# Performance work log

Measured on AMD Instinct MI355X. Metric: run time of the kernel, lower is better.

The kernel has to match this reference:

```python
import jax, jax.numpy as jnp
import numpy as np

MARGIN = 1.0
ALPHA = 0.5
EPS = 1e-12  # sqrt-smoothing epsilon (keeps grads finite on the zero diagonal)


def _pairwise_d2(x):
    # x: [B, D] -> squared euclidean distance matrix [B, B]
    sq = jnp.sum(x * x, axis=-1)
    return jnp.maximum(sq[:, None] + sq[None, :] - 2.0 * (x @ x.T), 0.0)


def setup_inputs() -> dict:
    key = jax.random.key(0)
    k1, k2 = jax.random.split(key)
    N, B, D = 32, 1024, 1024
    outputs = jax.random.normal(k1, (N, B, D), dtype=jnp.float32)
    encode_sentences = jax.random.normal(k2, (B, D), dtype=jnp.float32)
    return {"outputs": outputs, "encode_sentences": encode_sentences}


def reference(outputs, encode_sentences):
    # outputs: [N, B, D] (N secrets, batch B, embed D); encode_sentences: [B, D]
    N, B, D = outputs.shape

    # --- sentence (distance-consistency) loss ---
    # original: mean_i MSE( pdist(outputs[i]), pdist(encode_sentences) )
    d_sent = jnp.sqrt(_pairwise_d2(encode_sentences) + EPS)          # [B, B]
    d_out = jnp.sqrt(jax.vmap(_pairwise_d2)(outputs) + EPS)          # [N, B, B]
    # mean over N of per-i means == global mean (all terms same size B*B)
    sentence_loss = jnp.mean((d_out - d_sent[None]) ** 2)

    # --- secret (pairwise margin) loss ---
    # original: sum_{i<j} mean_b relu(margin - ||outputs[i,b] - outputs[j,b]||)
    x = jnp.swapaxes(outputs, 0, 1)                                   # [B, N, D]
    sq = jnp.sum(x * x, axis=-1)                                      # [B, N]
    gram = jnp.einsum('bnd,bmd->bnm', x, x)                           # [B, N, N]
    d2 = jnp.maximum(sq[:, :, None] + sq[:, None, :] - 2.0 * gram, 0.0)
    d = jnp.sqrt(d2 + EPS)                                            # [B, N, N]
    hinge = jax.nn.relu(MARGIN - d)                                   # [B, N, N]
    upper = jnp.triu(jnp.ones((N, N), dtype=bool), k=1)               # i < j mask
    secret_distance = jnp.sum(jnp.where(upper[None], hinge, 0.0)) / B
    n_pairs = N * (N - 1) / 2.0
    secret_loss = secret_distance / n_pairs

    loss = ALPHA * sentence_loss + (1.0 - ALPHA) * secret_loss
    return (loss, sentence_loss, secret_loss)
```

## Files before the change

kernel.cpp:

```cpp
#include <hip/hip_runtime.h>
#include <hip/hip_bf16.h>

#define N_SEC 32
#define BDIM 1024
#define DDIM 1024

typedef __attribute__((ext_vector_type(8))) short bf16x8;
typedef __attribute__((ext_vector_type(4))) float f32x4;
typedef __attribute__((ext_vector_type(4))) int i32x4;

#define WAITVM(n) asm volatile("s_waitcnt vmcnt(" #n ")" ::: "memory")

__device__ __forceinline__ void pipe_barrier() {
    __builtin_amdgcn_s_barrier();
    asm volatile("" ::: "memory");
    __builtin_amdgcn_sched_barrier(0);
}

__device__ __forceinline__ unsigned pk2(float a, float b) {
    union { __hip_bfloat162 h; unsigned u; } cv;
    cv.h = __float22bfloat162_rn(make_float2(a, b));
    return cv.u;
}

__device__ __forceinline__ i32x4 pack8(float4 a, float4 b) {
    i32x4 r;
    r[0] = pk2(a.x, a.y); r[1] = pk2(a.z, a.w);
    r[2] = pk2(b.x, b.y); r[3] = pk2(b.z, b.w);
    return r;
}

__device__ __forceinline__ f32x4 mfma16(bf16x8 a, bf16x8 b, f32x4 c) {
    return __builtin_amdgcn_mfma_f32_16x16x32_bf16(a, b, c, 0, 0, 0);
}

__device__ __forceinline__ float wave_sum(float v) {
    #pragma unroll
    for (int off = 32; off > 0; off >>= 1) v += __shfl_down(v, off, 64);
    return v;
}

__device__ __forceinline__ void gload16(const unsigned short* g, unsigned short* l) {
    __builtin_amdgcn_global_load_lds(
        (const __attribute__((address_space(1))) unsigned int*)g,
        (__attribute__((address_space(3))) unsigned int*)l, 16, 0, 0);
}


__global__ void prep_k(const float* __restrict__ outp, const float* __restrict__ enc,
                       unsigned short* __restrict__ Xb, unsigned short* __restrict__ Eb,
                       float* __restrict__ sq_out, float* __restrict__ sq_enc) {
    int wid = threadIdx.x >> 6, l = threadIdx.x & 63;
    int r = blockIdx.x * 4 + wid;
    bool isOut = r < N_SEC * BDIM;
    const float* src = isOut ? (outp + (size_t)r * DDIM)
                             : (enc + (size_t)(r - N_SEC * BDIM) * DDIM);
    unsigned short* dst = isOut ? (Xb + (size_t)r * DDIM)
                                : (Eb + (size_t)(r - N_SEC * BDIM) * DDIM);
    const float4* s4 = (const float4*)src;
    float s = 0.f;
    #pragma unroll
    for (int h = 0; h < 2; ++h) {
        int c = l + h * 64;
        float4 v0 = s4[2 * c], v1 = s4[2 * c + 1];
        i32x4 p = pack8(v0, v1);
        *(i32x4*)&dst[c * 8] = p;
        #pragma unroll
        for (int e = 0; e < 4; ++e) {
            unsigned u = (unsigned)p[e];
            float a = __uint_as_float(u << 16);
            float b = __uint_as_float(u & 0xFFFF0000u);
            s += a * a + b * b;
        }
    }
    s = wave_sum(s);
    if (l == 0) { if (isOut) sq_out[r] = s; else sq_enc[r - N_SEC * BDIM] = s; }
}

template<int MODE>
__global__ void gram5_k(const unsigned short* __restrict__ Xb, const float* __restrict__ sqv,
                        const float* __restrict__ dsent_r, float* __restrict__ dsent_w,
                        float* __restrict__ partials) {
    int n, tile;
    if (MODE == 1) {
        int g = blockIdx.x;
        int xcd = g & 7, local = g >> 3;
        n = xcd * 4 + local / 36;
        tile = local % 36;
    } else { n = 0; tile = blockIdx.x; }
    int idx = tile, ti = 0;
    while (idx >= 8 - ti) { idx -= 8 - ti; ti++; }
    int tj = ti + idx;
    const unsigned short* Xn = Xb + (size_t)n * BDIM * DDIM;
    const float* sqn = sqv + n * BDIM;
    int i0 = ti * 128, j0 = tj * 128;
    bool diag = (ti == tj);

    __shared__ __align__(16) unsigned short Ash[3][4096];
    __shared__ __align__(16) unsigned short Bsh[3][4096];
    __shared__ float red[4];

    int t = threadIdx.x, wid = t >> 6, l = t & 63;
    int wr = wid >> 1, wc = wid & 1;
    bool dead = diag && (wr > wc);
    int cg = l >> 4, lr = l & 15;

    f32x4 acc[4][4];
    #pragma unroll
    for (int a = 0; a < 4; a++)
        #pragma unroll
        for (int c = 0; c < 4; c++) acc[a][c] = f32x4{0.f, 0.f, 0.f, 0.f};

    int eoffA[4], eoffB[4];
    #pragma unroll
    for (int f = 0; f < 4; f++) {
        int ra = wr * 64 + f * 16 + lr;
        eoffA[f] = ra * 32 + ((cg ^ ((ra >> 1) & 3)) * 8);
        int rb = wc * 64 + f * 16 + lr;
        eoffB[f] = rb * 32 + ((cg ^ ((rb >> 1) & 3)) * 8);
    }

    int rs = wid * 16 + (l >> 2);
    int cgs = (l & 3) ^ ((rs >> 1) & 3);
    const unsigned short* gA0 = Xn + (size_t)(i0 + rs) * DDIM + cgs * 8;
    const unsigned short* gA1 = gA0 + (size_t)64 * DDIM;
    const unsigned short* gB0 = Xn + (size_t)(j0 + rs) * DDIM + cgs * 8;
    const unsigned short* gB1 = gB0 + (size_t)64 * DDIM;

    auto stage = [&](int buf, int kt) {
        int ko = kt * 32;
        gload16(gA0 + ko, &Ash[buf][wid * 512]);
        gload16(gA1 + ko, &Ash[buf][2048 + wid * 512]);
        gload16(gB0 + ko, &Bsh[buf][wid * 512]);
        gload16(gB1 + ko, &Bsh[buf][2048 + wid * 512]);
    };
    auto compute = [&](int buf) {
        if (dead) return;
        bf16x8 af[4], bfr[4];
        #pragma unroll
        for (int f = 0; f < 4; f++) {
            af[f]  = *(const bf16x8*)&Ash[buf][eoffA[f]];
            bfr[f] = *(const bf16x8*)&Bsh[buf][eoffB[f]];
        }
        #pragma unroll
        for (int fi = 0; fi < 4; fi++)
            #pragma unroll
            for (int fj = 0; fj < 4; fj++) {
                if (diag && wr == wc && fj < fi) continue;
                acc[fi][fj] = mfma16(af[fi], bfr[fj], acc[fi][fj]);
            }
    };

#define GSTEP(NB, CB) do {                       \
        pipe_barrier();                          \
        int nx = c + 2; if (nx > 31) nx = 31;    \
        stage(NB, nx);                           \
        WAITVM(8);                               \
        compute(CB);                             \
        ++c; } while (0)

    stage(0, 0); stage(1, 1);
    int c = 0;
    #pragma unroll 1
    for (int it = 0; it < 10; ++it) {
        GSTEP(2, 0);
        GSTEP(0, 1);
        GSTEP(1, 2);
    }
    GSTEP(2, 0);
    GSTEP(0, 1);
#undef GSTEP
    asm volatile("s_waitcnt vmcnt(0)" ::: "memory");

    float lsum = 0.f;
    if (!dead) {
        #pragma unroll
        for (int fi = 0; fi < 4; fi++) {
            #pragma unroll
            for (int fj = 0; fj < 4; fj++) {
                if (diag && wr == wc && fj < fi) continue;
                int jg = j0 + wc * 64 + fj * 16 + lr;
                #pragma unroll
                for (int e = 0; e < 4; e++) {
                    int ig = i0 + wr * 64 + fi * 16 + cg * 4 + e;
                    float g = acc[fi][fj][e];
                    float d2 = sqn[ig] + sqn[jg] - 2.f * g;
                    float d = sqrtf(fmaxf(d2, 0.f) + 1e-12f);
                    if (MODE == 0) {
                        dsent_w[(size_t)ig * BDIM + jg] = d;
                    } else {
                        if (!diag || jg > ig) {
                            float diff = d - dsent_r[(size_t)ig * BDIM + jg];
                            lsum += diff * diff;
                        }
                    }
                }
            }
        }
    }
    if (MODE == 1) {
        lsum = wave_sum(lsum * 2.f);
        if (l == 0) red[wid] = lsum;
        __syncthreads();
        if (t == 0) partials[blockIdx.x] = red[0] + red[1] + red[2] + red[3];
    }
}

__global__ void secret4_k(const unsigned short* __restrict__ Xb,
                          const float* __restrict__ sq_out, float* __restrict__ partials) {
    __shared__ __align__(16) unsigned short S[2][32 * 4 * 128];
    __shared__ float red[4];
    int t = threadIdx.x, wid = t >> 6, l = t & 63;
    int b0 = blockIdx.x * 4;
    int cg = l >> 4, lr = l & 15;
    f32x4 a00 = {0.f,0.f,0.f,0.f}, a01 = {0.f,0.f,0.f,0.f}, a11 = {0.f,0.f,0.f,0.f};

    auto stage = [&](int buf, int kt) {
        #pragma unroll
        for (int m = 0; m < 8; ++m) {
            int n = m * 4 + wid;
            gload16(Xb + ((size_t)(n * BDIM + b0 + cg)) * DDIM + kt * 128 + ((lr ^ (n & 7)) * 8),
                    &S[buf][n * 512]);
        }
    };
    auto compute = [&](int buf) {
        #pragma unroll
        for (int k2 = 0; k2 < 4; ++k2) {
            int cs = k2 * 4 + cg;
            int cl = (cs ^ (lr & 7)) * 8;
            bf16x8 u0 = *(const bf16x8*)&S[buf][lr * 512 + wid * 128 + cl];
            bf16x8 u1 = *(const bf16x8*)&S[buf][(16 + lr) * 512 + wid * 128 + cl];
            a00 = mfma16(u0, u0, a00);
            a01 = mfma16(u0, u1, a01);
            a11 = mfma16(u1, u1, a11);
        }
    };

    stage(0, 0);
    __syncthreads();
    for (int kt = 0; kt < 6; kt += 2) {
        stage(1, kt + 1);
        compute(0);
        __syncthreads();
        stage(0, kt + 2);
        compute(1);
        __syncthreads();
    }
    stage(1, 7);
    compute(0);
    __syncthreads();
    compute(1);

    float lsum = 0.f;
    int b = b0 + wid;
    auto proc = [&](const f32x4& acc, int rb, int cb) {
        #pragma unroll
        for (int e = 0; e < 4; e++) {
            int i = rb * 16 + cg * 4 + e;
            int j = cb * 16 + lr;
            if (j > i) {
                float d2 = sq_out[(size_t)i * BDIM + b] + sq_out[(size_t)j * BDIM + b] - 2.f * acc[e];
                float d = sqrtf(fmaxf(d2, 0.f) + 1e-12f);
                lsum += fmaxf(1.f - d, 0.f);
            }
        }
    };
    proc(a00, 0, 0); proc(a01, 0, 1); proc(a11, 1, 1);
    lsum = wave_sum(lsum);
    if (l == 0) red[wid] = lsum;
    __syncthreads();
    if (t == 0) partials[blockIdx.x] = red[0] + red[1] + red[2] + red[3];
}

__global__ void fin2_k(const float* __restrict__ ps, const float* __restrict__ psec,
                       float* __restrict__ out) {
    __shared__ float red[16];
    int t = threadIdx.x;
    float s = 0.f;
    for (int i = t; i < 36 * N_SEC; i += 256) s += ps[i];
    float s2 = psec[t];
    s = wave_sum(s);
    s2 = wave_sum(s2);
    if ((t & 63) == 0) { red[t >> 6] = s; red[8 + (t >> 6)] = s2; }
    __syncthreads();
    if (t == 0) {
        float a = red[0] + red[1] + red[2] + red[3];
        float b = red[8] + red[9] + red[10] + red[11];
        float sl = a * (1.0f / 33554432.0f);
        float sec = b * (1.0f / (1024.0f * 496.0f));
        out[0] = 0.5f * sl + 0.5f * sec;
        out[1] = sl;
        out[2] = sec;
    }
}


__global__ void norms_k(const float* __restrict__ outp, const float* __restrict__ enc,
                        float* __restrict__ sq_out, float* __restrict__ sq_enc) {
    int wid = threadIdx.x >> 6, l = threadIdx.x & 63;
    int r = blockIdx.x * 4 + wid;
    const float* src = (r < N_SEC * BDIM) ? (outp + (size_t)r * DDIM)
                                          : (enc + (size_t)(r - N_SEC * BDIM) * DDIM);
    float s = 0.f;
    #pragma unroll
    for (int q = 0; q < 4; q++) {
        float4 v = reinterpret_cast<const float4*>(src)[l + q * 64];
        unsigned u0 = pk2(v.x, v.y), u1 = pk2(v.z, v.w);
        float a = __uint_as_float(u0 << 16), b = __uint_as_float(u0 & 0xFFFF0000u);
        float c = __uint_as_float(u1 << 16), d = __uint_as_float(u1 & 0xFFFF0000u);
        s += a * a + b * b + c * c + d * d;
    }
    s = wave_sum(s);
    if (l == 0) { if (r < N_SEC * BDIM) sq_out[r] = s; else sq_enc[r - N_SEC * BDIM] = s; }
}

template<int MODE>
__global__ void gram_k(const float* __restrict__ X, const float* __restrict__ sqv,
                       const float* __restrict__ dsent_r, float* __restrict__ dsent_w,
                       float* __restrict__ accum) {
    int idx = blockIdx.x, ti = 0;
    while (idx >= 8 - ti) { idx -= 8 - ti; ti++; }
    int tj = ti + idx;
    int n = (MODE == 1) ? blockIdx.y : 0;
    const float* Xn = X + (size_t)n * BDIM * DDIM;
    const float* sqn = sqv + n * BDIM;
    int i0 = ti * 128, j0 = tj * 128;
    bool diag = (ti == tj);
    __shared__ __align__(16) unsigned short Ash[128 * 32];
    __shared__ __align__(16) unsigned short Bsh[128 * 32];
    int t = threadIdx.x, wid = t >> 6, l = t & 63;
    int wr = wid >> 1, wc = wid & 1;
    bool dead = diag && (wr > wc);
    int cg = l >> 4, lr = l & 15;
    f32x4 acc[4][4];
    #pragma unroll
    for (int a = 0; a < 4; a++)
        #pragma unroll
        for (int c = 0; c < 4; c++) acc[a][c] = f32x4{0.f, 0.f, 0.f, 0.f};
    int r0 = t >> 2, c0 = t & 3;
    int swz0 = (c0 ^ (r0 & 3)) * 8;
    int off0 = r0 * 32 + swz0;
    int off1 = (r0 + 64) * 32 + swz0;
    for (int kt = 0; kt < DDIM / 32; ++kt) {
        int k0 = kt * 32;
        const float4* pa0 = (const float4*)(Xn + (size_t)(i0 + r0) * DDIM + k0 + c0 * 8);
        const float4* pa1 = (const float4*)(Xn + (size_t)(i0 + r0 + 64) * DDIM + k0 + c0 * 8);
        const float4* pb0 = (const float4*)(Xn + (size_t)(j0 + r0) * DDIM + k0 + c0 * 8);
        const float4* pb1 = (const float4*)(Xn + (size_t)(j0 + r0 + 64) * DDIM + k0 + c0 * 8);
        float4 a00 = pa0[0], a01 = pa0[1];
        float4 a10 = pa1[0], a11 = pa1[1];
        float4 b00 = pb0[0], b01 = pb0[1];
        float4 b10 = pb1[0], b11 = pb1[1];
        __syncthreads();
        *(i32x4*)&Ash[off0] = pack8(a00, a01);
        *(i32x4*)&Ash[off1] = pack8(a10, a11);
        *(i32x4*)&Bsh[off0] = pack8(b00, b01);
        *(i32x4*)&Bsh[off1] = pack8(b10, b11);
        __syncthreads();
        if (!dead) {
            bf16x8 af[4], bfr[4];
            #pragma unroll
            for (int f = 0; f < 4; f++) {
                int ra = wr * 64 + f * 16 + lr;
                af[f] = *(const bf16x8*)&Ash[ra * 32 + ((cg ^ (ra & 3)) * 8)];
                int rb = wc * 64 + f * 16 + lr;
                bfr[f] = *(const bf16x8*)&Bsh[rb * 32 + ((cg ^ (rb & 3)) * 8)];
            }
            #pragma unroll
            for (int fi = 0; fi < 4; fi++)
                #pragma unroll
                for (int fj = 0; fj < 4; fj++) {
                    if (diag && wr == wc && fj < fi) continue;
                    acc[fi][fj] = mfma16(af[fi], bfr[fj], acc[fi][fj]);
                }
        }
    }
    if (!dead) {
        float lsum = 0.f;
        #pragma unroll
        for (int fi = 0; fi < 4; fi++) {
            #pragma unroll
            for (int fj = 0; fj < 4; fj++) {
                if (diag && wr == wc && fj < fi) continue;
                int jg = j0 + wc * 64 + fj * 16 + lr;
                #pragma unroll
                for (int e = 0; e < 4; e++) {
                    int ig = i0 + wr * 64 + fi * 16 + cg * 4 + e;
                    float g = acc[fi][fj][e];
                    float d2 = sqn[ig] + sqn[jg] - 2.f * g;
                    float d = sqrtf(fmaxf(d2, 0.f) + 1e-12f);
                    if (MODE == 0) {
                        dsent_w[(size_t)ig * BDIM + jg] = d;
                    } else {
                        if (!diag || jg > ig) {
                            float diff = d - dsent_r[(size_t)ig * BDIM + jg];
                            lsum += diff * diff;
                        }
                    }
                }
            }
        }
        if (MODE == 1) {
            lsum = wave_sum(lsum * 2.f);
            if (l == 0) atomicAdd(accum, lsum);
        }
    }
}

__global__ void secret_k(const float* __restrict__ X, const float* __restrict__ sq_out,
                         float* __restrict__ accum) {
    int wid = threadIdx.x >> 6, l = threadIdx.x & 63;
    int b = blockIdx.x * 4 + wid;
    int cg = l >> 4, lr = l & 15;
    f32x4 a00 = {0.f,0.f,0.f,0.f}, a01 = {0.f,0.f,0.f,0.f}, a11 = {0.f,0.f,0.f,0.f};
    for (int kt = 0; kt < 32; ++kt) {
        int k0 = kt * 32 + cg * 8;
        const float4* p0 = (const float4*)(X + ((size_t)lr * BDIM + b) * DDIM + k0);
        const float4* p1 = (const float4*)(X + ((size_t)(16 + lr) * BDIM + b) * DDIM + k0);
        union { i32x4 i; bf16x8 s; } u0, u1;
        u0.i = pack8(p0[0], p0[1]);
        u1.i = pack8(p1[0], p1[1]);
        a00 = mfma16(u0.s, u0.s, a00);
        a01 = mfma16(u0.s, u1.s, a01);
        a11 = mfma16(u1.s, u1.s, a11);
    }
    float lsum = 0.f;
    auto proc = [&](const f32x4& acc, int rb, int cb) {
        #pragma unroll
        for (int e = 0; e < 4; e++) {
            int i = rb * 16 + cg * 4 + e;
            int j = cb * 16 + lr;
            if (j > i) {
                float d2 = sq_out[(size_t)i * BDIM + b] + sq_out[(size_t)j * BDIM + b] - 2.f * acc[e];
                float d = sqrtf(fmaxf(d2, 0.f) + 1e-12f);
                lsum += fmaxf(1.f - d, 0.f);
            }
        }
    };
    proc(a00, 0, 0); proc(a01, 0, 1); proc(a11, 1, 1);
    lsum = wave_sum(lsum);
    if (l == 0) atomicAdd(accum, lsum);
}

__global__ void init_k(float* sums) { sums[threadIdx.x] = 0.f; }

__global__ void fin_k(const float* __restrict__ sums, float* __restrict__ out) {
    float sl = sums[0] * (1.0f / 33554432.0f);
    float sec = sums[1] * (1.0f / (1024.0f * 496.0f));
    out[0] = 0.5f * sl + 0.5f * sec;
    out[1] = sl;
    out[2] = sec;
}

extern "C" void kernel_launch(void* const* d_in, const int* in_sizes, int n_in,
                              void* d_out, int out_size, void* d_ws, size_t ws_size,
                              hipStream_t stream) {
    const float* outputs = (const float*)d_in[0];
    const float* enc     = (const float*)d_in[1];
    float* out = (float*)d_out;

    float* ps     = (float*)d_ws;
    float* psec   = ps + 1536;
    float* sq_out = ps + 2048;
    float* sq_enc = sq_out + N_SEC * BDIM;
    float* dsent  = sq_enc + BDIM;
    unsigned short* Xbf = (unsigned short*)(dsent + (size_t)BDIM * BDIM);
    unsigned short* Ebf = Xbf + (size_t)N_SEC * BDIM * DDIM;

    const size_t NEED = 4 * (2048 + (size_t)N_SEC * BDIM + BDIM + (size_t)BDIM * BDIM)
                      + 2 * ((size_t)N_SEC * BDIM * DDIM + (size_t)BDIM * DDIM);

    if (ws_size >= NEED) {
        hipLaunchKernelGGL(prep_k, dim3((N_SEC * BDIM + BDIM) / 4), dim3(256), 0, stream,
                           outputs, enc, Xbf, Ebf, sq_out, sq_enc);
        hipLaunchKernelGGL((gram5_k<0>), dim3(36), dim3(256), 0, stream,
                           Ebf, sq_enc, (const float*)nullptr, dsent, (float*)nullptr);
        hipLaunchKernelGGL((gram5_k<1>), dim3(36 * N_SEC), dim3(256), 0, stream,
                           Xbf, sq_out, (const float*)dsent, (float*)nullptr, ps);
        hipLaunchKernelGGL(secret4_k, dim3(BDIM / 4), dim3(256), 0, stream,
                           Xbf, sq_out, psec);
        hipLaunchKernelGGL(fin2_k, dim3(1), dim3(256), 0, stream, ps, psec, out);
    } else {
        float* sums = (float*)d_ws;
        float* fsq_out = sums + 64;
        float* fsq_enc = fsq_out + N_SEC * BDIM;
        float* fdsent  = fsq_enc + BDIM;
        hipLaunchKernelGGL(init_k, dim3(1), dim3(2), 0, stream, sums);
        hipLaunchKernelGGL(norms_k, dim3((N_SEC * BDIM + BDIM) / 4), dim3(256), 0, stream,
                           outputs, enc, fsq_out, fsq_enc);
        hipLaunchKernelGGL((gram_k<0>), dim3(36), dim3(256), 0, stream,
                           enc, fsq_enc, (const float*)nullptr, fdsent, (float*)nullptr);
        hipLaunchKernelGGL((gram_k<1>), dim3(36, N_SEC), dim3(256), 0, stream,
                           outputs, fsq_out, (const float*)fdsent, (float*)nullptr, &sums[0]);
        hipLaunchKernelGGL(secret_k, dim3(BDIM / 4), dim3(256), 0, stream,
                           outputs, fsq_out, &sums[1]);
        hipLaunchKernelGGL(fin_k, dim3(1), dim3(1), 0, stream, sums, out);
    }
}
```

Baseline: 153.0 us.

## Enlarge gram tiles to 256x256 with 8 waves and MFMA priority boost

Rewrites the pairwise-distance gram kernel to compute 256x256 upper-triangle tiles (10 per matrix) with 512-thread blocks, each wave holding a 128x64 accumulator, instead of 128x128 tiles (36 per matrix) with 256 threads. Larger tiles cut the repeated global/LDS loading of operand rows and the per-tile overhead. Diagonal-block skipping becomes finer-grained, and the MFMA section is wrapped in s_setprio. In exchange it uses more registers and LDS per block and launches only 320 blocks, so the GPU may be less evenly filled, and the last wave of blocks may be imbalanced.

```diff
diff --git a/kernel.cpp b/kernel.cpp
--- a/kernel.cpp
+++ b/kernel.cpp
@@ -78,85 +78,98 @@
 }
 
 template<int MODE>
-__global__ void gram5_k(const unsigned short* __restrict__ Xb, const float* __restrict__ sqv,
-                        const float* __restrict__ dsent_r, float* __restrict__ dsent_w,
-                        float* __restrict__ partials) {
+__global__ __launch_bounds__(512, 2)
+void gram7_k(const unsigned short* __restrict__ Xb, const float* __restrict__ sqv,
+             const float* __restrict__ dsent_r, float* __restrict__ dsent_w,
+             float* __restrict__ partials) {
     int n, tile;
     if (MODE == 1) {
         int g = blockIdx.x;
         int xcd = g & 7, local = g >> 3;
-        n = xcd * 4 + local / 36;
-        tile = local % 36;
+        n = xcd * 4 + local / 10;
+        tile = local % 10;
     } else { n = 0; tile = blockIdx.x; }
     int idx = tile, ti = 0;
-    while (idx >= 8 - ti) { idx -= 8 - ti; ti++; }
+    while (idx >= 4 - ti) { idx -= 4 - ti; ti++; }
     int tj = ti + idx;
     const unsigned short* Xn = Xb + (size_t)n * BDIM * DDIM;
     const float* sqn = sqv + n * BDIM;
-    int i0 = ti * 128, j0 = tj * 128;
+    int i0 = ti * 256, j0 = tj * 256;
     bool diag = (ti == tj);
 
-    __shared__ __align__(16) unsigned short Ash[3][4096];
-    __shared__ __align__(16) unsigned short Bsh[3][4096];
-    __shared__ float red[4];
+    __shared__ __align__(16) unsigned short Ash[3][8192];
+    __shared__ __align__(16) unsigned short Bsh[3][8192];
+    __shared__ float red[8];
 
     int t = threadIdx.x, wid = t >> 6, l = t & 63;
-    int wr = wid >> 1, wc = wid & 1;
-    bool dead = diag && (wr > wc);
+    int wr = wid >> 2, wc = wid & 3;
+    bool dead = diag && (wr == 1) && (wc < 2);
     int cg = l >> 4, lr = l & 15;
 
-    f32x4 acc[4][4];
-    #pragma unroll
-    for (int a = 0; a < 4; a++)
+    f32x4 acc[8][4];
+    #pragma unroll
+    for (int a = 0; a < 8; a++)
         #pragma unroll
         for (int c = 0; c < 4; c++) acc[a][c] = f32x4{0.f, 0.f, 0.f, 0.f};
 
-    int eoffA[4], eoffB[4];
+    int eoffA[8], eoffB[4];
+    #pragma unroll
+    for (int f = 0; f < 8; f++) {
+        int ra = wr * 128 + f * 16 + lr;
+        eoffA[f] = ra * 32 + ((cg ^ ((ra >> 1) & 3)) * 8);
+    }
     #pragma unroll
     for (int f = 0; f < 4; f++) {
-        int ra = wr * 64 + f * 16 + lr;
-        eoffA[f] = ra * 32 + ((cg ^ ((ra >> 1) & 3)) * 8);
         int rb = wc * 64 + f * 16 + lr;
         eoffB[f] = rb * 32 + ((cg ^ ((rb >> 1) & 3)) * 8);
     }
 
-    int rs = wid * 16 + (l >> 2);
-    int cgs = (l & 3) ^ ((rs >> 1) & 3);
-    const unsigned short* gA0 = Xn + (size_t)(i0 + rs) * DDIM + cgs * 8;
-    const unsigned short* gA1 = gA0 + (size_t)64 * DDIM;
-    const unsigned short* gB0 = Xn + (size_t)(j0 + rs) * DDIM + cgs * 8;
-    const unsigned short* gB1 = gB0 + (size_t)64 * DDIM;
+    int rs = t >> 2;
+    int cs = (t & 3) ^ ((rs >> 1) & 3);
+    const unsigned short* gA0 = Xn + (size_t)(i0 + rs) * DDIM + cs * 8;
+    const unsigned short* gA1 = gA0 + (size_t)128 * DDIM;
+    const unsigned short* gB0 = Xn + (size_t)(j0 + rs) * DDIM + cs * 8;
+    const unsigned short* gB1 = gB0 + (size_t)128 * DDIM;
 
     auto stage = [&](int buf, int kt) {
         int ko = kt * 32;
         gload16(gA0 + ko, &Ash[buf][wid * 512]);
-        gload16(gA1 + ko, &Ash[buf][2048 + wid * 512]);
+        gload16(gA1 + ko, &Ash[buf][4096 + wid * 512]);
         gload16(gB0 + ko, &Bsh[buf][wid * 512]);
-        gload16(gB1 + ko, &Bsh[buf][2048 + wid * 512]);
+        gload16(gB1 + ko, &Bsh[buf][4096 + wid * 512]);
     };
-    auto compute = [&](int buf) {
+    auto computeIter = [&](int buf) {
         if (dead) return;
-        bf16x8 af[4], bfr[4];
-        #pragma unroll
-        for (int f = 0; f < 4; f++) {
-            af[f]  = *(const bf16x8*)&Ash[buf][eoffA[f]];
-            bfr[f] = *(const bf16x8*)&Bsh[buf][eoffB[f]];
-        }
-        #pragma unroll
-        for (int fi = 0; fi < 4; fi++)
-            #pragma unroll
-            for (int fj = 0; fj < 4; fj++) {
-                if (diag && wr == wc && fj < fi) continue;
-                acc[fi][fj] = mfma16(af[fi], bfr[fj], acc[fi][fj]);
+        bf16x8 bfr[4];
+        #pragma unroll
+        for (int f = 0; f < 4; f++) bfr[f] = *(const bf16x8*)&Bsh[buf][eoffB[f]];
+        #pragma unroll
+        for (int q = 0; q < 2; ++q) {
+            bf16x8 af[4];
+            #pragma unroll
+            for (int f = 0; f < 4; f++)
+                af[f] = *(const bf16x8*)&Ash[buf][eoffA[q * 4 + f]];
+            __builtin_amdgcn_s_setprio(1);
+            #pragma unroll
+            for (int f = 0; f < 4; f++) {
+                int fi = q * 4 + f;
+                #pragma unroll
+                for (int fj = 0; fj < 4; fj++) {
+                    if (diag && (wc * 64 + fj * 16 + 15) < (wr * 128 + fi * 16))
+                        continue;
+                    acc[fi][fj] = mfma16(af[f], bfr[fj], acc[fi][fj]);
+                }
             }
+            __builtin_amdgcn_s_setprio(0);
+        }
     };
 
-#define GSTEP(NB, CB) do {                       \
+#define GSTEP(SB, CB) do {                       \
         pipe_barrier();                          \
         int nx = c + 2; if (nx > 31) nx = 31;    \
-        stage(NB, nx);                           \
+        stage(SB, nx);                           \
         WAITVM(8);                               \
-        compute(CB);                             \
+        computeIter(CB);                         \
         ++c; } while (0)
 
     stage(0, 0); stage(1, 1);
@@ -175,14 +188,15 @@
     float lsum = 0.f;
     if (!dead) {
         #pragma unroll
-        for (int fi = 0; fi < 4; fi++) {
+        for (int fi = 0; fi < 8; fi++) {
             #pragma unroll
             for (int fj = 0; fj < 4; fj++) {
-                if (diag && wr == wc && fj < fi) continue;
+                if (diag && (wc * 64 + fj * 16 + 15) < (wr * 128 + fi * 16))
+                    continue;
                 int jg = j0 + wc * 64 + fj * 16 + lr;
                 #pragma unroll
                 for (int e = 0; e < 4; e++) {
-                    int ig = i0 + wr * 64 + fi * 16 + cg * 4 + e;
+                    int ig = i0 + wr * 128 + fi * 16 + cg * 4 + e;
                     float g = acc[fi][fj][e];
                     float d2 = sqn[ig] + sqn[jg] - 2.f * g;
                     float d = sqrtf(fmaxf(d2, 0.f) + 1e-12f);
@@ -202,7 +216,12 @@
         lsum = wave_sum(lsum * 2.f);
         if (l == 0) red[wid] = lsum;
         __syncthreads();
-        if (t == 0) partials[blockIdx.x] = red[0] + red[1] + red[2] + red[3];
+        if (t == 0) {
+            float s = 0.f;
+            #pragma unroll
+            for (int w = 0; w < 8; ++w) s += red[w];
+            partials[blockIdx.x] = s;
+        }
     }
 }
 
@@ -277,7 +296,7 @@
     __shared__ float red[16];
     int t = threadIdx.x;
     float s = 0.f;
-    for (int i = t; i < 36 * N_SEC; i += 256) s += ps[i];
+    for (int i = t; i < 10 * N_SEC; i += 256) s += ps[i];
     float s2 = psec[t];
     s = wave_sum(s);
     s2 = wave_sum(s2);
@@ -473,9 +492,9 @@
     if (ws_size >= NEED) {
         hipLaunchKernelGGL(prep_k, dim3((N_SEC * BDIM + BDIM) / 4), dim3(256), 0, stream,
                            outputs, enc, Xbf, Ebf, sq_out, sq_enc);
-        hipLaunchKernelGGL((gram5_k<0>), dim3(36), dim3(256), 0, stream,
+        hipLaunchKernelGGL((gram7_k<0>), dim3(10), dim3(512), 0, stream,
                            Ebf, sq_enc, (const float*)nullptr, dsent, (float*)nullptr);
-        hipLaunchKernelGGL((gram5_k<1>), dim3(36 * N_SEC), dim3(256), 0, stream,
+        hipLaunchKernelGGL((gram7_k<1>), dim3(10 * N_SEC), dim3(512), 0, stream,
                            Xbf, sq_out, (const float*)dsent, (float*)nullptr, ps);
         hipLaunchKernelGGL(secret4_k, dim3(BDIM / 4), dim3(256), 0, stream,
                            Xbf, sq_out, psec);
```

Result: slower. 384.6 us (+151.4%).
